# Optimization experiments

Measured on AMD Instinct MI355X. Metric: run time of the kernel, lower is better.

The kernel has to match this reference:

```python
import jax, jax.numpy as jnp
import numpy as np

# Dims (match init_kwargs): N=81 driving series (perfect square -> zero padding path),
# M=64 encoder LSTM units, P=64 decoder LSTM units, T=128 timesteps, pred_len=1.
N, M, P, T, PRED = 81, 64, 64, 128, 1
SQ = 9                # sqrt(N): mtrx_row = mtrx_col = square_size = 9
C = SQ - 2 + 1        # conv_output_size = square_size - CNN_kernel + 1 = 8
B = 512


def _lstm_cell(x, h, c, Wih, Whh, bih, bhh):
    # torch.nn.LSTMCell: gates order i, f, g, o
    g = x @ Wih.T + bih + h @ Whh.T + bhh
    i, f, gg, o = jnp.split(g, 4, axis=1)
    c = jax.nn.sigmoid(f) * c + jax.nn.sigmoid(i) * jnp.tanh(gg)
    h = jax.nn.sigmoid(o) * jnp.tanh(c)
    return h, c


def setup_inputs():
    key = jax.random.key(0)
    ks = jax.random.split(key, 26)
    def rn(i, shape, s=0.1):
        return jax.random.normal(ks[i], shape, dtype=jnp.float32) * s
    return {
        'X_history': jax.random.normal(ks[0], (B, T, N), dtype=jnp.float32),
        'y_history': jax.random.normal(ks[1], (B, T, 1), dtype=jnp.float32),
        'conv_w': rn(2, (M, 1, 2, SQ)), 'conv_b': rn(3, (M,)),
        'We_w': rn(4, (T, 2 * M)), 'We_b': rn(5, (T,)),
        'Ue_w': rn(6, (T, C)),
        've_w': rn(7, (1, T)),
        'enc_Wih': rn(8, (4 * M, C)), 'enc_Whh': rn(9, (4 * M, M)),
        'enc_bih': rn(10, (4 * M,)), 'enc_bhh': rn(11, (4 * M,)),
        'Wd_w': rn(12, (M, 2 * P)), 'Wd_b': rn(13, (M,)),
        'Ud_w': rn(14, (M, M)),
        'vd_w': rn(15, (1, M)),
        'wt_w': rn(16, (1, M + 1)), 'wt_b': rn(17, (1,)),
        'dec_Wih': rn(18, (4 * P, 1)), 'dec_Whh': rn(19, (4 * P, P)),
        'dec_bih': rn(20, (4 * P,)), 'dec_bhh': rn(21, (4 * P,)),
        'Wy_w': rn(22, (P, P + M)), 'Wy_b': rn(23, (P,)),
        'vy_w': rn(24, (PRED, P)), 'vy_b': rn(25, (PRED,)),
    }


def _forward(X_history, y_history, conv_w, conv_b, We_w, We_b, Ue_w, ve_w,
             enc_Wih, enc_Whh, enc_bih, enc_bhh, Wd_w, Wd_b, Ud_w, vd_w,
             wt_w, wt_b, dec_Wih, dec_Whh, dec_bih, dec_bhh, Wy_w, Wy_b, vy_w, vy_b):
    Bv = X_history.shape[0]
    dt = X_history.dtype
    # ---- encoder CNN (state-independent -> hoisted out of the time loop) ----
    # N=81 is a perfect square: c = inputs[:,t,:].reshape(B,1,9,9), no padding.
    imgs = X_history.reshape(Bv, T, SQ, SQ)
    K = conv_w[:, 0]  # (M, 2, SQ); kernel width == image width -> per-row dot product
    conv = (jnp.einsum('btrw,mw->btmr', imgs[:, :, : SQ - 1, :], K[:, 0])
            + jnp.einsum('btrw,mw->btmr', imgs[:, :, 1:, :], K[:, 1])
            + conv_b[None, None, :, None])
    conv = jax.nn.relu(conv)  # (B, T, M, C); dropout is identity in eval

    # ---- encoder: input attention + LSTMCell recurrence over T ----
    def enc_step(carry, c_t):  # c_t: (B, M, C)
        h, s = carry
        x = jnp.concatenate([h, s], axis=1) @ We_w.T + We_b      # (B, T)
        z = jnp.tanh(x[:, None, :] + c_t @ Ue_w.T)               # (B, M, T)
        e = (z @ ve_w.T)[:, :, 0]                                # (B, M)
        alpha = jax.nn.softmax(e, axis=1)
        w_in = jnp.einsum('bm,bmc->bc', alpha, c_t)              # (B, C)
        h, s = _lstm_cell(w_in, h, s, enc_Wih, enc_Whh, enc_bih, enc_bhh)
        return (h, s), h

    h0 = jnp.zeros((Bv, M), dt)
    _, hs = jax.lax.scan(jax.checkpoint(enc_step), (h0, h0), jnp.swapaxes(conv, 0, 1))
    encoded = jnp.swapaxes(hs, 0, 1)  # (B, T, M)

    # ---- decoder: temporal attention + LSTMCell recurrence over T ----
    Uenc = encoded @ Ud_w.T  # loop-invariant U_d(encoded_inputs), (B, T, M)

    def dec_step(carry, y_t):  # y_t: (B, 1)
        d, sp = carry
        x1 = jnp.concatenate([d, sp], axis=1) @ Wd_w.T + Wd_b    # (B, M)
        z1 = jnp.tanh(x1[:, None, :] + Uenc)                     # (B, T, M)
        l = z1 @ vd_w.T                                          # (B, T, 1)
        beta = jax.nn.softmax(l, axis=1)
        c_t = jnp.sum(beta * encoded, axis=1)                    # (B, M)
        y_tilda = jnp.concatenate([c_t, y_t], axis=1) @ wt_w.T + wt_b
        d, sp = _lstm_cell(y_tilda, d, sp, dec_Wih, dec_Whh, dec_bih, dec_bhh)
        return (d, sp), c_t

    d0 = jnp.zeros((Bv, P), dt)
    (d, _), cts = jax.lax.scan(jax.checkpoint(dec_step), (d0, d0), jnp.swapaxes(y_history, 0, 1))
    c_last = cts[-1]
    out = (jnp.concatenate([d, c_last], axis=1) @ Wy_w.T + Wy_b) @ vy_w.T + vy_b
    return out  # (B, pred_len)


def reference(X_history, y_history, conv_w, conv_b, We_w, We_b, Ue_w, ve_w,
              enc_Wih, enc_Whh, enc_bih, enc_bhh, Wd_w, Wd_b, Ud_w, vd_w,
              wt_w, wt_b, dec_Wih, dec_Whh, dec_bih, dec_bhh, Wy_w, Wy_b, vy_w, vy_b):
    return _forward(X_history, y_history, conv_w, conv_b, We_w, We_b, Ue_w, ve_w,
                    enc_Wih, enc_Whh, enc_bih, enc_bhh, Wd_w, Wd_b, Ud_w, vd_w,
                    wt_w, wt_b, dec_Wih, dec_Whh, dec_bih, dec_bhh, Wy_w, Wy_b, vy_w, vy_b)
```

## Files before the change

kernel.cpp:

```cpp
#include <hip/hip_runtime.h>


#define TSTEPS 128

#define ENC   0
#define UENC  8192
#define CTL   16896
#define UEL   17664
#define XV    18688
#define HSB   18944
#define GBUF  19072
#define RED   19328
#define IMG   19424
#define WIB   19508
#define CTV   19516
#define LBUF  19580
#define TYP   19708
#define SMEMF 19772

__device__ __forceinline__ float rcpf(float x) { return __builtin_amdgcn_rcpf(x); }
__device__ __forceinline__ float fsigm(float x) { return rcpf(1.0f + __expf(-x)); }
__device__ __forceinline__ float ftanh(float x) { return 1.0f - 2.0f * rcpf(1.0f + __expf(2.0f * x)); }

__global__ __launch_bounds__(256, 2) void dstp_kernel(
    const float* __restrict__ Xh,   const float* __restrict__ yh,
    const float* __restrict__ convw,const float* __restrict__ convb,
    const float* __restrict__ Wew,  const float* __restrict__ Web,
    const float* __restrict__ Uew,  const float* __restrict__ vew,
    const float* __restrict__ eWih, const float* __restrict__ eWhh,
    const float* __restrict__ ebih, const float* __restrict__ ebhh,
    const float* __restrict__ Wdw,  const float* __restrict__ Wdb,
    const float* __restrict__ Udw,  const float* __restrict__ vdw,
    const float* __restrict__ wtw,  const float* __restrict__ wtb,
    const float* __restrict__ dWih, const float* __restrict__ dWhh,
    const float* __restrict__ dbih, const float* __restrict__ dbhh,
    const float* __restrict__ Wyw,  const float* __restrict__ Wyb,
    const float* __restrict__ vyw,  const float* __restrict__ vyb,
    float* __restrict__ out)
{
    extern __shared__ float sm[];
    const int tid = threadIdx.x;
    const int b   = blockIdx.x;

    for (int i = tid; i < 1024; i += 256) sm[UEL + i] = Uew[i];
    if (tid < 128) { sm[XV + 128 + tid] = vew[tid]; sm[HSB + tid] = 0.0f; }
    __syncthreads();

    const int dm = tid >> 2, dq = tid & 3;

    for (int t = 0; t < TSTEPS; ++t) {
        if (tid < 81) sm[IMG + tid] = Xh[((size_t)b * TSTEPS + t) * 81 + tid];
        {
            int j = tid >> 1, h = tid & 1;
            const float4* wr = reinterpret_cast<const float4*>(Wew + j * 128 + h * 64);
            const float4* hv = reinterpret_cast<const float4*>(sm + HSB + h * 64);
            float acc = 0.0f;
#pragma unroll
            for (int k = 0; k < 16; ++k) {
                float4 w = wr[k], x = hv[k];
                acc = fmaf(w.x, x.x, acc); acc = fmaf(w.y, x.y, acc);
                acc = fmaf(w.z, x.z, acc); acc = fmaf(w.w, x.w, acc);
            }
            acc += __shfl_xor(acc, 1);
            if (h == 0) sm[XV + j] = acc + Web[j];
        }
        __syncthreads();
#pragma unroll
        for (int rep = 0; rep < 2; ++rep) {
            int idx = tid + rep * 256;
            int m = idx >> 3, r = idx & 7;
            const float* kw = convw + m * 18;
            float acc = convb[m];
#pragma unroll
            for (int w = 0; w < 9; ++w) {
                acc = fmaf(sm[IMG + r * 9 + w],     kw[w],     acc);
                acc = fmaf(sm[IMG + r * 9 + 9 + w], kw[9 + w], acc);
            }
            sm[CTL + m * 12 + r] = fmaxf(acc, 0.0f);
        }
        __syncthreads();
        {
            const float4 c0 = *reinterpret_cast<const float4*>(sm + CTL + dm * 12);
            const float4 c1 = *reinterpret_cast<const float4*>(sm + CTL + dm * 12 + 4);
            float eacc = 0.0f;
#pragma unroll 8
            for (int jj = 0; jj < 32; ++jj) {
                int j = (jj << 2) | dq;
                float xj  = sm[XV + j];
                float vej = sm[XV + 128 + j];
                const float4 u0 = *reinterpret_cast<const float4*>(sm + UEL + j * 8);
                const float4 u1 = *reinterpret_cast<const float4*>(sm + UEL + j * 8 + 4);
                float s = xj;
                s = fmaf(u0.x, c0.x, s); s = fmaf(u0.y, c0.y, s);
                s = fmaf(u0.z, c0.z, s); s = fmaf(u0.w, c0.w, s);
                s = fmaf(u1.x, c1.x, s); s = fmaf(u1.y, c1.y, s);
                s = fmaf(u1.z, c1.z, s); s = fmaf(u1.w, c1.w, s);
                eacc = fmaf(ftanh(s), vej, eacc);
            }
            eacc += __shfl_xor(eacc, 1);
            eacc += __shfl_xor(eacc, 2);
            if (dq == 0) sm[RED + dm] = eacc;
        }
        __syncthreads();
        if (tid < 64) {
            float e = sm[RED + tid];
            float mx = e;
#pragma unroll
            for (int dd = 1; dd < 64; dd <<= 1) mx = fmaxf(mx, __shfl_xor(mx, dd));
            float ex = __expf(e - mx);
            float s = ex;
#pragma unroll
            for (int dd = 1; dd < 64; dd <<= 1) s += __shfl_xor(s, dd);
            float al = ex * rcpf(s);
            float p[8];
#pragma unroll
            for (int c = 0; c < 8; ++c) p[c] = al * sm[CTL + tid * 12 + c];
#pragma unroll
            for (int dd = 1; dd < 64; dd <<= 1) {
#pragma unroll
                for (int c = 0; c < 8; ++c) p[c] += __shfl_xor(p[c], dd);
            }
            if (tid == 0) {
#pragma unroll
                for (int c = 0; c < 8; ++c) sm[WIB + c] = p[c];
            }
        }
        __syncthreads();
        {
            const float4* wih = reinterpret_cast<const float4*>(eWih + tid * 8);
            float4 a0 = wih[0], a1 = wih[1];
            const float4 w0 = *reinterpret_cast<const float4*>(sm + WIB);
            const float4 w1 = *reinterpret_cast<const float4*>(sm + WIB + 4);
            float acc = ebih[tid] + ebhh[tid];
            acc = fmaf(a0.x, w0.x, acc); acc = fmaf(a0.y, w0.y, acc);
            acc = fmaf(a0.z, w0.z, acc); acc = fmaf(a0.w, w0.w, acc);
            acc = fmaf(a1.x, w1.x, acc); acc = fmaf(a1.y, w1.y, acc);
            acc = fmaf(a1.z, w1.z, acc); acc = fmaf(a1.w, w1.w, acc);
            const float4* whh = reinterpret_cast<const float4*>(eWhh + tid * 64);
            const float4* hv  = reinterpret_cast<const float4*>(sm + HSB);
#pragma unroll
            for (int k = 0; k < 16; ++k) {
                float4 w = whh[k], x = hv[k];
                acc = fmaf(w.x, x.x, acc); acc = fmaf(w.y, x.y, acc);
                acc = fmaf(w.z, x.z, acc); acc = fmaf(w.w, x.w, acc);
            }
            sm[GBUF + tid] = acc;
        }
        __syncthreads();
        if (tid < 64) {
            float gi = sm[GBUF + tid],       gf = sm[GBUF + 64 + tid];
            float gg = sm[GBUF + 128 + tid], go = sm[GBUF + 192 + tid];
            float c = fsigm(gf) * sm[HSB + 64 + tid] + fsigm(gi) * ftanh(gg);
            float h = fsigm(go) * ftanh(c);
            sm[HSB + tid] = h;
            sm[HSB + 64 + tid] = c;
            sm[ENC + t * 64 + tid] = h;
        }
        __syncthreads();
        {
            int j = tid >> 2, q = tid & 3;
            const float4* ud = reinterpret_cast<const float4*>(Udw + j * 64 + q * 16);
            const float4* hv = reinterpret_cast<const float4*>(sm + HSB + q * 16);
            float acc = 0.0f;
#pragma unroll
            for (int k = 0; k < 4; ++k) {
                float4 w = ud[k], x = hv[k];
                acc = fmaf(w.x, x.x, acc); acc = fmaf(w.y, x.y, acc);
                acc = fmaf(w.z, x.z, acc); acc = fmaf(w.w, x.w, acc);
            }
            acc += __shfl_xor(acc, 1);
            acc += __shfl_xor(acc, 2);
            if (q == 0) sm[UENC + t * 68 + j] = acc;
        }
        __syncthreads();
    }

    if (tid < 64) sm[UEL + tid] = vdw[tid];
    if (tid < 65) sm[UEL + 64 + tid] = wtw[tid];
    sm[UEL + 192 + tid] = dWih[tid];
    sm[UEL + 448 + tid] = dbih[tid] + dbhh[tid];
    if (tid < 64) sm[UEL + 704 + tid] = Wdb[tid];
    if (tid < 64) sm[UEL + 768 + tid] = Wyb[tid];
    if (tid < 64) sm[UEL + 832 + tid] = vyw[tid];
    if (tid < 128) sm[HSB + tid] = 0.0f;
    __syncthreads();

    for (int t = 0; t < TSTEPS; ++t) {
        {
            int j = tid >> 2, q = tid & 3;
            const float4* wd = reinterpret_cast<const float4*>(Wdw + j * 128 + q * 32);
            const float4* dv = reinterpret_cast<const float4*>(sm + HSB + q * 32);
            float acc = 0.0f;
#pragma unroll
            for (int k = 0; k < 8; ++k) {
                float4 w = wd[k], x = dv[k];
                acc = fmaf(w.x, x.x, acc); acc = fmaf(w.y, x.y, acc);
                acc = fmaf(w.z, x.z, acc); acc = fmaf(w.w, x.w, acc);
            }
            acc += __shfl_xor(acc, 1);
            acc += __shfl_xor(acc, 2);
            if (q == 0) sm[XV + j] = acc + sm[UEL + 704 + j];
        }
        __syncthreads();
        {
            int tt2 = tid >> 1, h = tid & 1;
            const float* ur = sm + UENC + tt2 * 68 + h * 32;
            const float* xr = sm + XV + h * 32;
            const float* vr = sm + UEL + h * 32;
            float acc = 0.0f;
#pragma unroll
            for (int j4 = 0; j4 < 8; ++j4) {
                float4 u = *reinterpret_cast<const float4*>(ur + j4 * 4);
                float4 x = *reinterpret_cast<const float4*>(xr + j4 * 4);
                float4 v = *reinterpret_cast<const float4*>(vr + j4 * 4);
                acc = fmaf(ftanh(x.x + u.x), v.x, acc);
                acc = fmaf(ftanh(x.y + u.y), v.y, acc);
                acc = fmaf(ftanh(x.z + u.z), v.z, acc);
                acc = fmaf(ftanh(x.w + u.w), v.w, acc);
            }
            acc += __shfl_xor(acc, 1);
            if (h == 0) sm[LBUF + tt2] = acc;
        }
        __syncthreads();
        if (tid < 64) {
            float v0 = sm[LBUF + tid], v1 = sm[LBUF + 64 + tid];
            float mx = fmaxf(v0, v1);
#pragma unroll
            for (int dd = 1; dd < 64; dd <<= 1) mx = fmaxf(mx, __shfl_xor(mx, dd));
            float e0 = __expf(v0 - mx), e1 = __expf(v1 - mx);
            float s = e0 + e1;
#pragma unroll
            for (int dd = 1; dd < 64; dd <<= 1) s += __shfl_xor(s, dd);
            float r = rcpf(s);
            sm[LBUF + tid] = e0 * r;
            sm[LBUF + 64 + tid] = e1 * r;
        }
        __syncthreads();
        {
            int j = tid & 63, q = tid >> 6;
            float acc = 0.0f;
#pragma unroll 8
            for (int i = 0; i < 32; ++i) {
                int ttk = (q << 5) + i;
                acc = fmaf(sm[LBUF + ttk], sm[ENC + ttk * 64 + j], acc);
            }
            sm[GBUF + tid] = acc;
        }
        __syncthreads();
        if (tid < 64) {
            float cv = sm[GBUF + tid] + sm[GBUF + 64 + tid] +
                       sm[GBUF + 128 + tid] + sm[GBUF + 192 + tid];
            sm[CTV + tid] = cv;
            float p = cv * sm[UEL + 64 + tid];
#pragma unroll
            for (int dd = 1; dd < 64; dd <<= 1) p += __shfl_xor(p, dd);
            if (tid == 0)
                sm[RED + 64] = p + yh[(size_t)b * TSTEPS + t] * sm[UEL + 128] + wtb[0];
        }
        __syncthreads();
        {
            float yt = sm[RED + 64];
            float acc = fmaf(yt, sm[UEL + 192 + tid], sm[UEL + 448 + tid]);
            const float4* whh = reinterpret_cast<const float4*>(dWhh + tid * 64);
            const float4* dv  = reinterpret_cast<const float4*>(sm + HSB);
#pragma unroll
            for (int k = 0; k < 16; ++k) {
                float4 w = whh[k], x = dv[k];
                acc = fmaf(w.x, x.x, acc); acc = fmaf(w.y, x.y, acc);
                acc = fmaf(w.z, x.z, acc); acc = fmaf(w.w, x.w, acc);
            }
            sm[GBUF + tid] = acc;
        }
        __syncthreads();
        if (tid < 64) {
            float gi = sm[GBUF + tid],       gf = sm[GBUF + 64 + tid];
            float gg = sm[GBUF + 128 + tid], go = sm[GBUF + 192 + tid];
            float c = fsigm(gf) * sm[HSB + 64 + tid] + fsigm(gi) * ftanh(gg);
            float dnew = fsigm(go) * ftanh(c);
            sm[HSB + tid] = dnew;
            sm[HSB + 64 + tid] = c;
        }
        __syncthreads();
    }

    {
        int p = tid >> 2, q = tid & 3;
        const float4* wy = reinterpret_cast<const float4*>(Wyw + p * 128 + q * 32);
        const float4* sv = reinterpret_cast<const float4*>(
            (q < 2) ? (sm + HSB + q * 32) : (sm + CTV + (q - 2) * 32));
        float acc = 0.0f;
#pragma unroll
        for (int k = 0; k < 8; ++k) {
            float4 w = wy[k], x = sv[k];
            acc = fmaf(w.x, x.x, acc); acc = fmaf(w.y, x.y, acc);
            acc = fmaf(w.z, x.z, acc); acc = fmaf(w.w, x.w, acc);
        }
        acc += __shfl_xor(acc, 1);
        acc += __shfl_xor(acc, 2);
        if (q == 0) sm[TYP + p] = acc + sm[UEL + 768 + p];
    }
    __syncthreads();
    if (tid < 64) {
        float v = sm[TYP + tid] * sm[UEL + 832 + tid];
#pragma unroll
        for (int dd = 1; dd < 64; dd <<= 1) v += __shfl_xor(v, dd);
        if (tid == 0) out[b] = v + vyb[0];
    }
}

extern "C" void kernel_launch(void* const* d_in, const int* in_sizes, int n_in,
                              void* d_out, int out_size, void* d_ws, size_t ws_size,
                              hipStream_t stream) {
    const float* A[26];
    for (int i = 0; i < 26; ++i) A[i] = (const float*)d_in[i];
    (void)in_sizes; (void)n_in; (void)d_ws; (void)ws_size; (void)out_size;

    (void)hipFuncSetAttribute(reinterpret_cast<const void*>(dstp_kernel),
                              hipFuncAttributeMaxDynamicSharedMemorySize,
                              SMEMF * 4);

    dstp_kernel<<<dim3(512), dim3(256), SMEMF * 4, stream>>>(
        A[0], A[1], A[2], A[3], A[4], A[5], A[6], A[7], A[8], A[9],
        A[10], A[11], A[12], A[13], A[14], A[15], A[16], A[17], A[18], A[19],
        A[20], A[21], A[22], A[23], A[24], A[25], (float*)d_out);
}
```

Measured before the change: 1.283 ms.

## Double block to 512 threads, batch Uenc projection, and cut per-step barriers

Raises the block size to 512 threads and re-partitions every per-timestep stage to use them. The encoder input-attention softmax and weighted sum now run redundantly in every wavefront, with results kept in registers, which removes a barrier and the shared-memory round trip. The per-step Ud·h projection is taken out of the encoder loop and computed once afterwards as a small batched matmul over all encoder states. In the decoder, the Whh·d matvec is issued before the context reduction barrier so the two overlap, and y_history plus the small constants are staged in LDS. The costs are more threads per block, higher register pressure from launch_bounds(512,4), and duplicated softmax work across the 8 wavefronts.

New measurement: 3.358 ms. 162% more time.

```diff
diff --git a/kernel.cpp b/kernel.cpp
--- a/kernel.cpp
+++ b/kernel.cpp
@@ -3,26 +3,41 @@
 
 #define TSTEPS 128
 
-#define ENC   0
-#define UENC  8192
-#define CTL   16896
-#define UEL   17664
-#define XV    18688
-#define HSB   18944
-#define GBUF  19072
-#define RED   19328
-#define IMG   19424
-#define WIB   19508
-#define CTV   19516
-#define LBUF  19580
-#define TYP   19708
-#define SMEMF 19772
+#define ENC    0
+#define UENC   8192
+#define UE     16896
+#define CTL    17920
+#define XVE    18432
+#define HSB    18688
+#define GBUF   18816
+#define RED    19328
+#define REDS   19840
+#define IMG    19848
+#define CTV    19932
+#define LBUF   19996
+#define SMEMF  20124
+
+#define DC_VD    16896
+#define DC_WT    16960
+#define DC_DWIH  17152
+#define DC_DBIAS 17408
+#define DC_WDB   17664
+#define DC_WYB   17728
+#define DC_VY    17792
+#define DC_SC    17856
+#define DC_YH    17920
+#define GB2      19328
+#define TYP      19848
 
 __device__ __forceinline__ float rcpf(float x) { return __builtin_amdgcn_rcpf(x); }
 __device__ __forceinline__ float fsigm(float x) { return rcpf(1.0f + __expf(-x)); }
 __device__ __forceinline__ float ftanh(float x) { return 1.0f - 2.0f * rcpf(1.0f + __expf(2.0f * x)); }
 
-__global__ __launch_bounds__(256, 2) void dstp_kernel(
+#define FMA4(d_, p_, q_) \
+    d_ = fmaf((p_).x, (q_).x, d_); d_ = fmaf((p_).y, (q_).y, d_); \
+    d_ = fmaf((p_).z, (q_).z, d_); d_ = fmaf((p_).w, (q_).w, d_);
+
+__global__ __launch_bounds__(512, 4) void dstp_kernel(
     const float* __restrict__ Xh,   const float* __restrict__ yh,
     const float* __restrict__ convw,const float* __restrict__ convb,
     const float* __restrict__ Wew,  const float* __restrict__ Web,
@@ -42,33 +57,26 @@
     const int tid = threadIdx.x;
     const int b   = blockIdx.x;
 
-    for (int i = tid; i < 1024; i += 256) sm[UEL + i] = Uew[i];
-    if (tid < 128) { sm[XV + 128 + tid] = vew[tid]; sm[HSB + tid] = 0.0f; }
+    for (int i = tid; i < 1024; i += 512) sm[UE + i] = Uew[i];
+    if (tid < 128) { sm[XVE + tid * 2 + 1] = vew[tid]; sm[HSB + tid] = 0.0f; }
     __syncthreads();
-
-    const int dm = tid >> 2, dq = tid & 3;
 
     for (int t = 0; t < TSTEPS; ++t) {
         if (tid < 81) sm[IMG + tid] = Xh[((size_t)b * TSTEPS + t) * 81 + tid];
         {
-            int j = tid >> 1, h = tid & 1;
-            const float4* wr = reinterpret_cast<const float4*>(Wew + j * 128 + h * 64);
-            const float4* hv = reinterpret_cast<const float4*>(sm + HSB + h * 64);
-            float acc = 0.0f;
-#pragma unroll
-            for (int k = 0; k < 16; ++k) {
-                float4 w = wr[k], x = hv[k];
-                acc = fmaf(w.x, x.x, acc); acc = fmaf(w.y, x.y, acc);
-                acc = fmaf(w.z, x.z, acc); acc = fmaf(w.w, x.w, acc);
-            }
+            int j = tid >> 2, q = tid & 3;
+            const float4* wr = reinterpret_cast<const float4*>(Wew + j * 128 + q * 32);
+            const float4* hv = reinterpret_cast<const float4*>(sm + HSB + q * 32);
+            float acc = 0.0f;
+#pragma unroll
+            for (int k = 0; k < 8; ++k) { float4 wv = wr[k], xv = hv[k]; FMA4(acc, wv, xv) }
             acc += __shfl_xor(acc, 1);
-            if (h == 0) sm[XV + j] = acc + Web[j];
-        }
-        __syncthreads();
-#pragma unroll
-        for (int rep = 0; rep < 2; ++rep) {
-            int idx = tid + rep * 256;
-            int m = idx >> 3, r = idx & 7;
+            acc += __shfl_xor(acc, 2);
+            if (q == 0) sm[XVE + j * 2] = acc + Web[j];
+        }
+        __syncthreads();
+        {
+            int m = tid >> 3, r = tid & 7;
             const float* kw = convw + m * 18;
             float acc = convb[m];
 #pragma unroll
@@ -76,75 +84,67 @@
                 acc = fmaf(sm[IMG + r * 9 + w],     kw[w],     acc);
                 acc = fmaf(sm[IMG + r * 9 + 9 + w], kw[9 + w], acc);
             }
-            sm[CTL + m * 12 + r] = fmaxf(acc, 0.0f);
-        }
-        __syncthreads();
-        {
-            const float4 c0 = *reinterpret_cast<const float4*>(sm + CTL + dm * 12);
-            const float4 c1 = *reinterpret_cast<const float4*>(sm + CTL + dm * 12 + 4);
+            sm[CTL + m * 8 + r] = fmaxf(acc, 0.0f);
+        }
+        __syncthreads();
+        const int m = tid & 63;
+        const float4 c0 = *reinterpret_cast<const float4*>(sm + CTL + m * 8);
+        const float4 c1 = *reinterpret_cast<const float4*>(sm + CTL + m * 8 + 4);
+        {
+            int w = tid >> 6;
             float eacc = 0.0f;
-#pragma unroll 8
-            for (int jj = 0; jj < 32; ++jj) {
-                int j = (jj << 2) | dq;
-                float xj  = sm[XV + j];
-                float vej = sm[XV + 128 + j];
-                const float4 u0 = *reinterpret_cast<const float4*>(sm + UEL + j * 8);
-                const float4 u1 = *reinterpret_cast<const float4*>(sm + UEL + j * 8 + 4);
-                float s = xj;
-                s = fmaf(u0.x, c0.x, s); s = fmaf(u0.y, c0.y, s);
-                s = fmaf(u0.z, c0.z, s); s = fmaf(u0.w, c0.w, s);
-                s = fmaf(u1.x, c1.x, s); s = fmaf(u1.y, c1.y, s);
-                s = fmaf(u1.z, c1.z, s); s = fmaf(u1.w, c1.w, s);
-                eacc = fmaf(ftanh(s), vej, eacc);
-            }
-            eacc += __shfl_xor(eacc, 1);
-            eacc += __shfl_xor(eacc, 2);
-            if (dq == 0) sm[RED + dm] = eacc;
-        }
-        __syncthreads();
-        if (tid < 64) {
-            float e = sm[RED + tid];
+#pragma unroll
+            for (int jj = 0; jj < 16; ++jj) {
+                int j = w * 16 + jj;
+                float4 u0 = *reinterpret_cast<const float4*>(sm + UE + j * 8);
+                float4 u1 = *reinterpret_cast<const float4*>(sm + UE + j * 8 + 4);
+                float2 xv = *reinterpret_cast<const float2*>(sm + XVE + j * 2);
+                float s = xv.x;
+                FMA4(s, u0, c0) FMA4(s, u1, c1)
+                eacc = fmaf(ftanh(s), xv.y, eacc);
+            }
+            sm[RED + (tid >> 6) * 64 + m] = eacc;
+        }
+        __syncthreads();
+        float win[8];
+        {
+            float e = 0.0f;
+#pragma unroll
+            for (int p = 0; p < 8; ++p) e += sm[RED + p * 64 + m];
             float mx = e;
 #pragma unroll
             for (int dd = 1; dd < 64; dd <<= 1) mx = fmaxf(mx, __shfl_xor(mx, dd));
             float ex = __expf(e - mx);
-            float s = ex;
-#pragma unroll
-            for (int dd = 1; dd < 64; dd <<= 1) s += __shfl_xor(s, dd);
-            float al = ex * rcpf(s);
-            float p[8];
-#pragma unroll
-            for (int c = 0; c < 8; ++c) p[c] = al * sm[CTL + tid * 12 + c];
+            float ssum = ex;
+#pragma unroll
+            for (int dd = 1; dd < 64; dd <<= 1) ssum += __shfl_xor(ssum, dd);
+            float al = ex * rcpf(ssum);
+            win[0] = al * c0.x; win[1] = al * c0.y; win[2] = al * c0.z; win[3] = al * c0.w;
+            win[4] = al * c1.x; win[5] = al * c1.y; win[6] = al * c1.z; win[7] = al * c1.w;
 #pragma unroll
             for (int dd = 1; dd < 64; dd <<= 1) {
 #pragma unroll
-                for (int c = 0; c < 8; ++c) p[c] += __shfl_xor(p[c], dd);
-            }
-            if (tid == 0) {
-#pragma unroll
-                for (int c = 0; c < 8; ++c) sm[WIB + c] = p[c];
-            }
-        }
-        __syncthreads();
-        {
-            const float4* wih = reinterpret_cast<const float4*>(eWih + tid * 8);
-            float4 a0 = wih[0], a1 = wih[1];
-            const float4 w0 = *reinterpret_cast<const float4*>(sm + WIB);
-            const float4 w1 = *reinterpret_cast<const float4*>(sm + WIB + 4);
-            float acc = ebih[tid] + ebhh[tid];
-            acc = fmaf(a0.x, w0.x, acc); acc = fmaf(a0.y, w0.y, acc);
-            acc = fmaf(a0.z, w0.z, acc); acc = fmaf(a0.w, w0.w, acc);
-            acc = fmaf(a1.x, w1.x, acc); acc = fmaf(a1.y, w1.y, acc);
-            acc = fmaf(a1.z, w1.z, acc); acc = fmaf(a1.w, w1.w, acc);
-            const float4* whh = reinterpret_cast<const float4*>(eWhh + tid * 64);
-            const float4* hv  = reinterpret_cast<const float4*>(sm + HSB);
-#pragma unroll
-            for (int k = 0; k < 16; ++k) {
-                float4 w = whh[k], x = hv[k];
-                acc = fmaf(w.x, x.x, acc); acc = fmaf(w.y, x.y, acc);
-                acc = fmaf(w.z, x.z, acc); acc = fmaf(w.w, x.w, acc);
-            }
-            sm[GBUF + tid] = acc;
+                for (int c = 0; c < 8; ++c) win[c] += __shfl_xor(win[c], dd);
+            }
+        }
+        {
+            int j = tid >> 1, hk = tid & 1;
+            const float4* whh = reinterpret_cast<const float4*>(eWhh + j * 64 + hk * 32);
+            const float4* hv  = reinterpret_cast<const float4*>(sm + HSB + hk * 32);
+            float acc = 0.0f;
+#pragma unroll
+            for (int k = 0; k < 8; ++k) { float4 wv = whh[k], xv = hv[k]; FMA4(acc, wv, xv) }
+            acc += __shfl_xor(acc, 1);
+            if (hk == 0) {
+                const float4* wih = reinterpret_cast<const float4*>(eWih + j * 8);
+                float4 a0 = wih[0], a1 = wih[1];
+                float acc2 = ebih[j] + ebhh[j];
+                acc2 = fmaf(a0.x, win[0], acc2); acc2 = fmaf(a0.y, win[1], acc2);
+                acc2 = fmaf(a0.z, win[2], acc2); acc2 = fmaf(a0.w, win[3], acc2);
+                acc2 = fmaf(a1.x, win[4], acc2); acc2 = fmaf(a1.y, win[5], acc2);
+                acc2 = fmaf(a1.z, win[6], acc2); acc2 = fmaf(a1.w, win[7], acc2);
+                sm[GBUF + j] = acc + acc2;
+            }
         }
         __syncthreads();
         if (tid < 64) {
@@ -157,69 +157,68 @@
             sm[ENC + t * 64 + tid] = h;
         }
         __syncthreads();
-        {
-            int j = tid >> 2, q = tid & 3;
-            const float4* ud = reinterpret_cast<const float4*>(Udw + j * 64 + q * 16);
-            const float4* hv = reinterpret_cast<const float4*>(sm + HSB + q * 16);
-            float acc = 0.0f;
-#pragma unroll
-            for (int k = 0; k < 4; ++k) {
-                float4 w = ud[k], x = hv[k];
-                acc = fmaf(w.x, x.x, acc); acc = fmaf(w.y, x.y, acc);
-                acc = fmaf(w.z, x.z, acc); acc = fmaf(w.w, x.w, acc);
-            }
+    }
+
+    if (tid < 64)  sm[DC_VD + tid] = vdw[tid];
+    if (tid < 65)  sm[DC_WT + tid] = wtw[tid];
+    if (tid < 256) { sm[DC_DWIH + tid] = dWih[tid]; sm[DC_DBIAS + tid] = dbih[tid] + dbhh[tid]; }
+    if (tid < 64)  { sm[DC_WDB + tid] = Wdb[tid]; sm[DC_WYB + tid] = Wyb[tid]; sm[DC_VY + tid] = vyw[tid]; }
+    if (tid < 64)  sm[XVE + tid * 2 + 1] = vdw[tid];
+    if (tid < 128) { sm[HSB + tid] = 0.0f; sm[DC_YH + tid] = yh[(size_t)b * TSTEPS + tid]; }
+    if (tid == 0)  { sm[DC_SC] = wtb[0]; sm[DC_SC + 1] = vyb[0]; }
+    {
+        int j = tid >> 3, e8 = tid & 7;
+        float acc[16];
+#pragma unroll
+        for (int i = 0; i < 16; ++i) acc[i] = 0.0f;
+#pragma unroll
+        for (int kc = 0; kc < 4; ++kc) {
+            const float4* ud = reinterpret_cast<const float4*>(Udw + j * 64 + kc * 16);
+            float4 u0 = ud[0], u1 = ud[1], u2 = ud[2], u3 = ud[3];
+#pragma unroll
+            for (int i = 0; i < 16; ++i) {
+                const float4* er = reinterpret_cast<const float4*>(sm + ENC + (e8 * 16 + i) * 64 + kc * 16);
+                float4 e0 = er[0], e1 = er[1], e2 = er[2], e3 = er[3];
+                float a = acc[i];
+                FMA4(a, u0, e0) FMA4(a, u1, e1) FMA4(a, u2, e2) FMA4(a, u3, e3)
+                acc[i] = a;
+            }
+        }
+#pragma unroll
+        for (int i4 = 0; i4 < 4; ++i4) {
+            *reinterpret_cast<float4*>(sm + UENC + j * 136 + e8 * 16 + i4 * 4) =
+                make_float4(acc[i4 * 4], acc[i4 * 4 + 1], acc[i4 * 4 + 2], acc[i4 * 4 + 3]);
+        }
+    }
+    __syncthreads();
+
+    for (int t = 0; t < TSTEPS; ++t) {
+        {
+            int j = tid >> 3, o = tid & 7;
+            const float4* wd = reinterpret_cast<const float4*>(Wdw + j * 128 + o * 16);
+            const float4* dv = reinterpret_cast<const float4*>(sm + HSB + o * 16);
+            float acc = 0.0f;
+#pragma unroll
+            for (int k = 0; k < 4; ++k) { float4 wv = wd[k], xv = dv[k]; FMA4(acc, wv, xv) }
             acc += __shfl_xor(acc, 1);
             acc += __shfl_xor(acc, 2);
-            if (q == 0) sm[UENC + t * 68 + j] = acc;
-        }
-        __syncthreads();
-    }
-
-    if (tid < 64) sm[UEL + tid] = vdw[tid];
-    if (tid < 65) sm[UEL + 64 + tid] = wtw[tid];
-    sm[UEL + 192 + tid] = dWih[tid];
-    sm[UEL + 448 + tid] = dbih[tid] + dbhh[tid];
-    if (tid < 64) sm[UEL + 704 + tid] = Wdb[tid];
-    if (tid < 64) sm[UEL + 768 + tid] = Wyb[tid];
-    if (tid < 64) sm[UEL + 832 + tid] = vyw[tid];
-    if (tid < 128) sm[HSB + tid] = 0.0f;
-    __syncthreads();
-
-    for (int t = 0; t < TSTEPS; ++t) {
-        {
-            int j = tid >> 2, q = tid & 3;
-            const float4* wd = reinterpret_cast<const float4*>(Wdw + j * 128 + q * 32);
-            const float4* dv = reinterpret_cast<const float4*>(sm + HSB + q * 32);
-            float acc = 0.0f;
-#pragma unroll
-            for (int k = 0; k < 8; ++k) {
-                float4 w = wd[k], x = dv[k];
-                acc = fmaf(w.x, x.x, acc); acc = fmaf(w.y, x.y, acc);
-                acc = fmaf(w.z, x.z, acc); acc = fmaf(w.w, x.w, acc);
+            acc += __shfl_xor(acc, 4);
+            if (o == 0) sm[XVE + j * 2] = acc + sm[DC_WDB + j];
+        }
+        __syncthreads();
+        {
+            int tt = tid >> 2, q = tid & 3;
+            float acc = 0.0f;
+#pragma unroll
+            for (int jj = 0; jj < 16; ++jj) {
+                int j = jj * 4 + q;
+                float u = sm[UENC + j * 136 + tt];
+                float2 xv = *reinterpret_cast<const float2*>(sm + XVE + j * 2);
+                acc = fmaf(ftanh(xv.x + u), xv.y, acc);
             }
             acc += __shfl_xor(acc, 1);
             acc += __shfl_xor(acc, 2);
-            if (q == 0) sm[XV + j] = acc + sm[UEL + 704 + j];
-        }
-        __syncthreads();
-        {
-            int tt2 = tid >> 1, h = tid & 1;
-            const float* ur = sm + UENC + tt2 * 68 + h * 32;
-            const float* xr = sm + XV + h * 32;
-            const float* vr = sm + UEL + h * 32;
-            float acc = 0.0f;
-#pragma unroll
-            for (int j4 = 0; j4 < 8; ++j4) {
-                float4 u = *reinterpret_cast<const float4*>(ur + j4 * 4);
-                float4 x = *reinterpret_cast<const float4*>(xr + j4 * 4);
-                float4 v = *reinterpret_cast<const float4*>(vr + j4 * 4);
-                acc = fmaf(ftanh(x.x + u.x), v.x, acc);
-                acc = fmaf(ftanh(x.y + u.y), v.y, acc);
-                acc = fmaf(ftanh(x.z + u.z), v.z, acc);
-                acc = fmaf(ftanh(x.w + u.w), v.w, acc);
-            }
-            acc += __shfl_xor(acc, 1);
-            if (h == 0) sm[LBUF + tt2] = acc;
+            if (q == 0) sm[LBUF + tt] = acc;
         }
         __syncthreads();
         if (tid < 64) {
@@ -236,45 +235,49 @@
             sm[LBUF + 64 + tid] = e1 * r;
         }
         __syncthreads();
-        {
-            int j = tid & 63, q = tid >> 6;
-            float acc = 0.0f;
-#pragma unroll 8
-            for (int i = 0; i < 32; ++i) {
-                int ttk = (q << 5) + i;
+        float hacc = 0.0f;
+        {
+            int j = tid >> 1, hk = tid & 1;
+            const float4* whh = reinterpret_cast<const float4*>(dWhh + j * 64 + hk * 32);
+            const float4* dv  = reinterpret_cast<const float4*>(sm + HSB + hk * 32);
+#pragma unroll
+            for (int k = 0; k < 8; ++k) { float4 wv = whh[k], xv = dv[k]; FMA4(hacc, wv, xv) }
+        }
+        {
+            int j = tid & 63, cc = tid >> 6;
+            float acc = 0.0f;
+#pragma unroll
+            for (int i = 0; i < 16; ++i) {
+                int ttk = cc * 16 + i;
                 acc = fmaf(sm[LBUF + ttk], sm[ENC + ttk * 64 + j], acc);
             }
-            sm[GBUF + tid] = acc;
+            sm[GBUF + cc * 64 + j] = acc;
         }
         __syncthreads();
         if (tid < 64) {
-            float cv = sm[GBUF + tid] + sm[GBUF + 64 + tid] +
-                       sm[GBUF + 128 + tid] + sm[GBUF + 192 + tid];
+            float cv = 0.0f;
+#pragma unroll
+            for (int cc = 0; cc < 8; ++cc) cv += sm[GBUF + cc * 64 + tid];
             sm[CTV + tid] = cv;
-            float p = cv * sm[UEL + 64 + tid];
+            float p = cv * sm[DC_WT + tid];
 #pragma unroll
             for (int dd = 1; dd < 64; dd <<= 1) p += __shfl_xor(p, dd);
             if (tid == 0)
-                sm[RED + 64] = p + yh[(size_t)b * TSTEPS + t] * sm[UEL + 128] + wtb[0];
-        }
-        __syncthreads();
-        {
-            float yt = sm[RED + 64];
-            float acc = fmaf(yt, sm[UEL + 192 + tid], sm[UEL + 448 + tid]);
-            const float4* whh = reinterpret_cast<const float4*>(dWhh + tid * 64);
-            const float4* dv  = reinterpret_cast<const float4*>(sm + HSB);
-#pragma unroll
-            for (int k = 0; k < 16; ++k) {
-                float4 w = whh[k], x = dv[k];
-                acc = fmaf(w.x, x.x, acc); acc = fmaf(w.y, x.y, acc);
-                acc = fmaf(w.z, x.z, acc); acc = fmaf(w.w, x.w, acc);
-            }
-            sm[GBUF + tid] = acc;
+                sm[REDS] = p + sm[DC_YH + t] * sm[DC_WT + 64] + sm[DC_SC];
+        }
+        __syncthreads();
+        {
+            int j = tid >> 1, hk = tid & 1;
+            float acc = hacc + __shfl_xor(hacc, 1);
+            if (hk == 0) {
+                float yt = sm[REDS];
+                sm[GB2 + j] = acc + fmaf(yt, sm[DC_DWIH + j], sm[DC_DBIAS + j]);
+            }
         }
         __syncthreads();
         if (tid < 64) {
-            float gi = sm[GBUF + tid],       gf = sm[GBUF + 64 + tid];
-            float gg = sm[GBUF + 128 + tid], go = sm[GBUF + 192 + tid];
+            float gi = sm[GB2 + tid],       gf = sm[GB2 + 64 + tid];
+            float gg = sm[GB2 + 128 + tid], go = sm[GB2 + 192 + tid];
             float c = fsigm(gf) * sm[HSB + 64 + tid] + fsigm(gi) * ftanh(gg);
             float dnew = fsigm(go) * ftanh(c);
             sm[HSB + tid] = dnew;
@@ -284,27 +287,24 @@
     }
 
     {
-        int p = tid >> 2, q = tid & 3;
-        const float4* wy = reinterpret_cast<const float4*>(Wyw + p * 128 + q * 32);
+        int p = tid >> 3, o = tid & 7;
+        const float4* wy = reinterpret_cast<const float4*>(Wyw + p * 128 + o * 16);
         const float4* sv = reinterpret_cast<const float4*>(
-            (q < 2) ? (sm + HSB + q * 32) : (sm + CTV + (q - 2) * 32));
+            (o < 4) ? (sm + HSB + o * 16) : (sm + CTV + (o - 4) * 16));
         float acc = 0.0f;
 #pragma unroll
-        for (int k = 0; k < 8; ++k) {
-            float4 w = wy[k], x = sv[k];
-            acc = fmaf(w.x, x.x, acc); acc = fmaf(w.y, x.y, acc);
-            acc = fmaf(w.z, x.z, acc); acc = fmaf(w.w, x.w, acc);
-        }
+        for (int k = 0; k < 4; ++k) { float4 wv = wy[k], xv = sv[k]; FMA4(acc, wv, xv) }
         acc += __shfl_xor(acc, 1);
         acc += __shfl_xor(acc, 2);
-        if (q == 0) sm[TYP + p] = acc + sm[UEL + 768 + p];
+        acc += __shfl_xor(acc, 4);
+        if (o == 0) sm[TYP + p] = acc + sm[DC_WYB + p];
     }
     __syncthreads();
     if (tid < 64) {
-        float v = sm[TYP + tid] * sm[UEL + 832 + tid];
+        float v = sm[TYP + tid] * sm[DC_VY + tid];
 #pragma unroll
         for (int dd = 1; dd < 64; dd <<= 1) v += __shfl_xor(v, dd);
-        if (tid == 0) out[b] = v + vyb[0];
+        if (tid == 0) out[b] = v + sm[DC_SC + 1];
     }
 }
 
@@ -319,7 +319,7 @@
                               hipFuncAttributeMaxDynamicSharedMemorySize,
                               SMEMF * 4);
 
-    dstp_kernel<<<dim3(512), dim3(256), SMEMF * 4, stream>>>(
+    dstp_kernel<<<dim3(512), dim3(512), SMEMF * 4, stream>>>(
         A[0], A[1], A[2], A[3], A[4], A[5], A[6], A[7], A[8], A[9],
         A[10], A[11], A[12], A[13], A[14], A[15], A[16], A[17], A[18], A[19],
         A[20], A[21], A[22], A[23], A[24], A[25], (float*)d_out);
```
